# Performance work log

Hardware: AMD Instinct MI355X
Metric: run time of the kernel (lower is better)

## Reference

```python
import jax, jax.numpy as jnp
import numpy as np

N = 50000        # nodes
E = 800000       # edges (avg degree 16)
NODE_DIM = 64
HID = 64
OUT = 1
K = 2            # hops per TAGConv
P = 0.5          # dropout rate


def setup_inputs() -> dict:
    key = jax.random.key(0)
    ks = jax.random.split(key, 8)
    x = jax.random.normal(ks[0], (N, NODE_DIM), dtype=jnp.float32)
    edge_index = jax.random.randint(ks[1], (2, E), 0, N, dtype=jnp.int64)
    # positive edge weights (traffic-style), keeps degree normalization well-defined
    edge_attr = jax.random.uniform(ks[2], (E,), dtype=jnp.float32, minval=0.1, maxval=1.0)
    s = 0.1
    W0 = (jax.random.normal(ks[3], (K + 1, NODE_DIM, HID), dtype=jnp.float32) * s)
    W1 = (jax.random.normal(ks[4], (K + 1, HID, HID), dtype=jnp.float32) * s)
    W2 = (jax.random.normal(ks[5], (K + 1, HID, OUT), dtype=jnp.float32) * s)
    a0 = jnp.full((1,), 0.25, dtype=jnp.float32)  # PReLU slope (num_parameters=1)
    a1 = jnp.full((1,), 0.25, dtype=jnp.float32)
    return {"x": x, "edge_index": edge_index, "edge_attr": edge_attr,
            "W0": W0, "W1": W1, "W2": W2, "a0": a0, "a1": a1}


def _tagconv(x, row, col, norm, W):
    # out = sum_{k=0..K} (A_norm^k x) @ W[k]
    out = x @ W[0]
    h = x
    for k in range(1, K + 1):
        # gather source features, scale by edge norm, scatter-add to targets
        h = jax.ops.segment_sum(h[row] * norm[:, None], col, num_segments=N)
        out = out + h @ W[k]
    return out


def _dropout(h, key):
    keep = jax.random.bernoulli(key, 1.0 - P, h.shape)
    return jnp.where(keep, h / (1.0 - P), 0.0)


def _prelu(h, a):
    return jnp.where(h >= 0, h, a * h)


def reference(x, edge_index, edge_attr, W0, W1, W2, a0, a1):
    row, col = edge_index[0], edge_index[1]
    # symmetric GCN normalization (PyG TAGConv default, no added self-loops)
    deg = jax.ops.segment_sum(edge_attr, col, num_segments=N)
    dinv = jnp.where(deg > 0, jax.lax.rsqrt(jnp.maximum(deg, 1e-12)), 0.0)
    norm = dinv[row] * edge_attr * dinv[col]

    dk = jax.random.split(jax.random.key(42), 2)
    h = _tagconv(x, row, col, norm, W0)
    h = _prelu(_dropout(h, dk[0]), a0)
    h = _tagconv(h, row, col, norm, W1)
    h = _prelu(_dropout(h, dk[1]), a1)
    return _tagconv(h, row, col, norm, W2)
```

## Files before the change

kernel.cpp:

```cpp
#include <hip/hip_runtime.h>
#include <stdint.h>

#define N_NODES 50000
#define N_EDGES 800000
#define DIM 64
#define FEAT_TOTAL (N_NODES * DIM)
#define ELL_S 48
#define NB 200
#define BROWS 250
#define BCAP 6000
#define ECHUNK (N_EDGES / NB)
#define AST 200

typedef __attribute__((ext_vector_type(8))) short bf16x8;
typedef __attribute__((ext_vector_type(4))) float f32x4;

__device__ inline float bf2f(uint32_t h) { return __uint_as_float(h << 16); }
__device__ inline uint32_t f2bf(float f) {
  uint32_t u = __float_as_uint(f);
  return (u + 0x7fffu + ((u >> 16) & 1u)) >> 16;
}

__host__ __device__ inline void threefry2x32(uint32_t k0, uint32_t k1,
                                             uint32_t x0, uint32_t x1,
                                             uint32_t& o0, uint32_t& o1) {
  uint32_t ks[3] = {k0, k1, k0 ^ k1 ^ 0x1BD11BDAu};
  x0 += ks[0];
  x1 += ks[1];
  const uint32_t R[2][4] = {{13u, 15u, 26u, 6u}, {17u, 29u, 16u, 24u}};
#pragma unroll
  for (int g = 0; g < 5; ++g) {
    const uint32_t* r = R[g & 1];
#pragma unroll
    for (int j = 0; j < 4; ++j) {
      x0 += x1;
      x1 = (x1 << r[j]) | (x1 >> (32u - r[j]));
      x1 ^= x0;
    }
    x0 += ks[(g + 1) % 3];
    x1 += ks[(g + 2) % 3] + (uint32_t)(g + 1);
  }
  o0 = x0;
  o1 = x1;
}

__global__ __launch_bounds__(256) void phaseA(
    const int* __restrict__ row, const int* __restrict__ col,
    const float* __restrict__ w, int* __restrict__ bfill,
    int2* __restrict__ bkt, int E) {
  __shared__ int hist[NB], base[NB], off[NB];
  int t = threadIdx.x;
  int lo = blockIdx.x * ECHUNK;
  int hi = min(lo + ECHUNK, E);
  for (int i = t; i < NB; i += 256) hist[i] = 0;
  __syncthreads();
  for (int e = lo + t; e < hi; e += 256) atomicAdd(&hist[col[e] / BROWS], 1);
  __syncthreads();
  for (int i = t; i < NB; i += 256) {
    base[i] = atomicAdd(&bfill[i], hist[i]);
    off[i] = 0;
  }
  __syncthreads();
  for (int e = lo + t; e < hi; e += 256) {
    int c = col[e];
    int bin = c / BROWS;
    int rank = atomicAdd(&off[bin], 1);
    int dest = base[bin] + rank;
    if (dest < BCAP) {
      int2 ent;
      ent.x = row[e] | ((c - bin * BROWS) << 17);
      ent.y = __float_as_int(w[e]);
      bkt[(size_t)bin * BCAP + dest] = ent;
    }
  }
}

__global__ __launch_bounds__(256) void phaseC(
    const int* __restrict__ bfill, const int2* __restrict__ bkt,
    int2* __restrict__ ell, int* __restrict__ cnt, float* __restrict__ dinv) {
  __shared__ int lcnt[BROWS];
  __shared__ float ldeg[BROWS];
  int t = threadIdx.x;
  int b = blockIdx.x;
  for (int i = t; i < BROWS; i += 256) {
    lcnt[i] = 0;
    ldeg[i] = 0.0f;
  }
  __syncthreads();
  int sz = min(bfill[b], BCAP);
  const int2* src = bkt + (size_t)b * BCAP;
  for (int i = t; i < sz; i += 256) {
    int2 ent = src[i];
    int cl = (ent.x >> 17) & 0xff;
    int r = ent.x & 0x1ffff;
    float wv = __int_as_float(ent.y);
    int slot = atomicAdd(&lcnt[cl], 1);
    if (slot < ELL_S) {
      int2 o;
      o.x = r;
      o.y = ent.y;
      ell[(size_t)(b * BROWS + cl) * ELL_S + slot] = o;
    }
    atomicAdd(&ldeg[cl], wv);
  }
  __syncthreads();
  for (int i = t; i < BROWS; i += 256) {
    cnt[b * BROWS + i] = lcnt[i];
    float d = ldeg[i];
    dinv[b * BROWS + i] = (d > 0.0f) ? rsqrtf(fmaxf(d, 1e-12f)) : 0.0f;
  }
}

__global__ void normw_ell(int2* __restrict__ ell, const int* __restrict__ cnt,
                          const float* __restrict__ dinv, int n_nodes) {
  int gid = blockIdx.x * blockDim.x + threadIdx.x;
  int n = gid >> 6;
  if (n >= n_nodes) return;
  int lane = threadIdx.x & 63;
  int c = min(cnt[n], ELL_S);
  if (lane >= c) return;
  float dn = dinv[n];
  int2 ent = ell[(size_t)n * ELL_S + lane];
  ent.y = __float_as_int(dinv[ent.x] * __int_as_float(ent.y) * dn);
  ell[(size_t)n * ELL_S + lane] = ent;
}

__global__ void cvt_all(const float* __restrict__ x,
                        const float* __restrict__ W0,
                        const float* __restrict__ W1,
                        uint16_t* __restrict__ xb, uint16_t* __restrict__ Wt0,
                        uint16_t* __restrict__ Wt1) {
  int id = blockIdx.x * blockDim.x + threadIdx.x;
  if (id < FEAT_TOTAL) xb[id] = (uint16_t)f2bf(x[id]);
  if (id < 192 * DIM) {
    int kk = id >> 6;
    int j = id & 63;
    Wt0[j * 192 + kk] = (uint16_t)f2bf(W0[id]);
    Wt1[j * 192 + kk] = (uint16_t)f2bf(W1[id]);
  }
}

__global__ void prop_bf16(const uint16_t* __restrict__ src,
                          uint16_t* __restrict__ dst,
                          const int2* __restrict__ ell,
                          const int* __restrict__ cnt, int n_nodes) {
  int gid = blockIdx.x * blockDim.x + threadIdx.x;
  int n = gid >> 5;
  if (n >= n_nodes) return;
  int hl = threadIdx.x & 31;
  int eg = hl >> 3;
  int fc = hl & 7;
  int c = min(cnt[n], ELL_S);
  const int2* p = ell + (size_t)n * ELL_S;
  float acc[8] = {0.f, 0.f, 0.f, 0.f, 0.f, 0.f, 0.f, 0.f};
  int k = eg;
  for (; k + 4 < c; k += 8) {
    int2 e0 = p[k];
    int2 e1 = p[k + 4];
    float w0 = __int_as_float(e0.y);
    float w1 = __int_as_float(e1.y);
    uint4 v0 = *(const uint4*)&src[e0.x * DIM + fc * 8];
    uint4 v1 = *(const uint4*)&src[e1.x * DIM + fc * 8];
    acc[0] += bf2f(v0.x & 0xffffu) * w0 + bf2f(v1.x & 0xffffu) * w1;
    acc[1] += bf2f(v0.x >> 16) * w0 + bf2f(v1.x >> 16) * w1;
    acc[2] += bf2f(v0.y & 0xffffu) * w0 + bf2f(v1.y & 0xffffu) * w1;
    acc[3] += bf2f(v0.y >> 16) * w0 + bf2f(v1.y >> 16) * w1;
    acc[4] += bf2f(v0.z & 0xffffu) * w0 + bf2f(v1.z & 0xffffu) * w1;
    acc[5] += bf2f(v0.z >> 16) * w0 + bf2f(v1.z >> 16) * w1;
    acc[6] += bf2f(v0.w & 0xffffu) * w0 + bf2f(v1.w & 0xffffu) * w1;
    acc[7] += bf2f(v0.w >> 16) * w0 + bf2f(v1.w >> 16) * w1;
  }
  if (k < c) {
    int2 e0 = p[k];
    float w0 = __int_as_float(e0.y);
    uint4 v0 = *(const uint4*)&src[e0.x * DIM + fc * 8];
    acc[0] += bf2f(v0.x & 0xffffu) * w0;
    acc[1] += bf2f(v0.x >> 16) * w0;
    acc[2] += bf2f(v0.y & 0xffffu) * w0;
    acc[3] += bf2f(v0.y >> 16) * w0;
    acc[4] += bf2f(v0.z & 0xffffu) * w0;
    acc[5] += bf2f(v0.z >> 16) * w0;
    acc[6] += bf2f(v0.w & 0xffffu) * w0;
    acc[7] += bf2f(v0.w >> 16) * w0;
  }
#pragma unroll
  for (int m = 8; m <= 16; m <<= 1) {
#pragma unroll
    for (int j = 0; j < 8; ++j) acc[j] += __shfl_xor(acc[j], m);
  }
  if (eg == 0) {
    uint4 r;
    r.x = f2bf(acc[0]) | (f2bf(acc[1]) << 16);
    r.y = f2bf(acc[2]) | (f2bf(acc[3]) << 16);
    r.z = f2bf(acc[4]) | (f2bf(acc[5]) << 16);
    r.w = f2bf(acc[6]) | (f2bf(acc[7]) << 16);
    *(uint4*)&dst[(size_t)n * DIM + fc * 8] = r;
  }
}

__global__ void sprop_add_ell(const float* __restrict__ src,
                              const float* __restrict__ addv,
                              float* __restrict__ dst,
                              const int2* __restrict__ ell,
                              const int* __restrict__ cnt, int n_nodes) {
  int n = blockIdx.x * blockDim.x + threadIdx.x;
  if (n >= n_nodes) return;
  int c = min(cnt[n], ELL_S);
  const int2* p = ell + (size_t)n * ELL_S;
  float acc = addv[n];
  for (int k = 0; k < c; ++k)
    acc += __int_as_float(p[k].y) * src[p[k].x];
  dst[n] = acc;
}

__global__ __launch_bounds__(256) void gemm3_mfma_g(
    const uint16_t* X, const uint16_t* __restrict__ P1,
    const int2* __restrict__ ell, const int* __restrict__ cnt,
    const uint16_t* __restrict__ Wt, uint16_t* out, int n_nodes, uint32_t k0,
    uint32_t k1, const float* __restrict__ a) {
  __shared__ uint16_t sA[64 * AST];
  __shared__ uint16_t sB[64 * AST];
  int t = threadIdx.x;
  int n0 = blockIdx.x * 64;
#pragma unroll
  for (int m = 0; m < 2; ++m) {
    const uint16_t* S = (m == 0) ? X : P1;
#pragma unroll
    for (int it = 0; it < 2; ++it) {
      int chunk = t + it * 256;
      int rrow = chunk >> 3;
      int cc = chunk & 7;
      int nc = min(n0 + rrow, n_nodes - 1);
      uint4 v = *(const uint4*)&S[(size_t)nc * DIM + cc * 8];
      *(uint4*)&sA[rrow * AST + m * DIM + cc * 8] = v;
    }
  }
  {
    int wv = t >> 6;
    int lane = t & 63;
    int half = lane >> 5;
    int hl = lane & 31;
    int eg = hl >> 3;
    int fc = hl & 7;
#pragma unroll
    for (int i = 0; i < 8; ++i) {
      int ln = wv * 16 + i * 2 + half;
      int nc = min(n0 + ln, n_nodes - 1);
      int c = min(cnt[nc], ELL_S);
      const int2* p = ell + (size_t)nc * ELL_S;
      float acc[8] = {0.f, 0.f, 0.f, 0.f, 0.f, 0.f, 0.f, 0.f};
      int k = eg;
      for (; k + 4 < c; k += 8) {
        int2 e0 = p[k];
        int2 e1 = p[k + 4];
        float w0 = __int_as_float(e0.y);
        float w1 = __int_as_float(e1.y);
        uint4 v0 = *(const uint4*)&P1[e0.x * DIM + fc * 8];
        uint4 v1 = *(const uint4*)&P1[e1.x * DIM + fc * 8];
        acc[0] += bf2f(v0.x & 0xffffu) * w0 + bf2f(v1.x & 0xffffu) * w1;
        acc[1] += bf2f(v0.x >> 16) * w0 + bf2f(v1.x >> 16) * w1;
        acc[2] += bf2f(v0.y & 0xffffu) * w0 + bf2f(v1.y & 0xffffu) * w1;
        acc[3] += bf2f(v0.y >> 16) * w0 + bf2f(v1.y >> 16) * w1;
        acc[4] += bf2f(v0.z & 0xffffu) * w0 + bf2f(v1.z & 0xffffu) * w1;
        acc[5] += bf2f(v0.z >> 16) * w0 + bf2f(v1.z >> 16) * w1;
        acc[6] += bf2f(v0.w & 0xffffu) * w0 + bf2f(v1.w & 0xffffu) * w1;
        acc[7] += bf2f(v0.w >> 16) * w0 + bf2f(v1.w >> 16) * w1;
      }
      if (k < c) {
        int2 e0 = p[k];
        float w0 = __int_as_float(e0.y);
        uint4 v0 = *(const uint4*)&P1[e0.x * DIM + fc * 8];
        acc[0] += bf2f(v0.x & 0xffffu) * w0;
        acc[1] += bf2f(v0.x >> 16) * w0;
        acc[2] += bf2f(v0.y & 0xffffu) * w0;
        acc[3] += bf2f(v0.y >> 16) * w0;
        acc[4] += bf2f(v0.z & 0xffffu) * w0;
        acc[5] += bf2f(v0.z >> 16) * w0;
        acc[6] += bf2f(v0.w & 0xffffu) * w0;
        acc[7] += bf2f(v0.w >> 16) * w0;
      }
#pragma unroll
      for (int m = 8; m <= 16; m <<= 1) {
#pragma unroll
        for (int j = 0; j < 8; ++j) acc[j] += __shfl_xor(acc[j], m);
      }
      if (eg == 0) {
        uint4 r;
        r.x = f2bf(acc[0]) | (f2bf(acc[1]) << 16);
        r.y = f2bf(acc[2]) | (f2bf(acc[3]) << 16);
        r.z = f2bf(acc[4]) | (f2bf(acc[5]) << 16);
        r.w = f2bf(acc[6]) | (f2bf(acc[7]) << 16);
        *(uint4*)&sA[ln * AST + 2 * DIM + fc * 8] = r;
      }
    }
  }
#pragma unroll
  for (int it = 0; it < 6; ++it) {
    int chunk = t + it * 256;
    int rrow = chunk / 24;
    int cc = chunk % 24;
    uint4 v = *(const uint4*)&Wt[rrow * 192 + cc * 8];
    *(uint4*)&sB[rrow * AST + cc * 8] = v;
  }
  __syncthreads();
  int wv = t >> 6;
  int lane = t & 63;
  int lm = lane & 15;
  int quad = lane >> 4;
  f32x4 acc[4] = {};
  const uint16_t* pB = &sB[(wv * 16 + lm) * AST + quad * 8];
  const uint16_t* pA = &sA[lm * AST + quad * 8];
#pragma unroll
  for (int ks = 0; ks < 6; ++ks) {
    bf16x8 bf = *(const bf16x8*)(pB + ks * 32);
#pragma unroll
    for (int rt = 0; rt < 4; ++rt) {
      bf16x8 af = *(const bf16x8*)(pA + rt * 16 * AST + ks * 32);
      acc[rt] = __builtin_amdgcn_mfma_f32_16x16x32_bf16(af, bf, acc[rt], 0, 0, 0);
    }
  }
  float al = a[0];
  int col = wv * 16 + lm;
#pragma unroll
  for (int rt = 0; rt < 4; ++rt) {
#pragma unroll
    for (int r = 0; r < 4; ++r) {
      int n = n0 + rt * 16 + quad * 4 + r;
      if (n < n_nodes) {
        float v = acc[rt][r];
        uint32_t idx = (uint32_t)(n * DIM + col);
        uint32_t o0, o1;
        threefry2x32(k0, k1, 0u, idx, o0, o1);
        v = ((o0 ^ o1) & 0x80000000u) ? 0.0f : (v + v);
        v = (v >= 0.0f) ? v : al * v;
        out[(size_t)n * DIM + col] = (uint16_t)f2bf(v);
      }
    }
  }
}

__global__ void matvec3_bf16(const uint16_t* __restrict__ F,
                             const float* __restrict__ W2,
                             float* __restrict__ y0, float* __restrict__ y1,
                             float* __restrict__ y2, int n_nodes) {
  int gid = blockIdx.x * blockDim.x + threadIdx.x;
  int n = gid >> 6;
  int i = gid & 63;
  if (n >= n_nodes) return;
  float v = bf2f((uint32_t)F[(size_t)n * DIM + i]);
  float s0 = v * W2[i], s1 = v * W2[DIM + i], s2 = v * W2[2 * DIM + i];
#pragma unroll
  for (int off = 32; off > 0; off >>= 1) {
    s0 += __shfl_down(s0, off);
    s1 += __shfl_down(s1, off);
    s2 += __shfl_down(s2, off);
  }
  if (i == 0) {
    y0[n] = s0;
    y1[n] = s1;
    y2[n] = s2;
  }
}

extern "C" void kernel_launch(void* const* d_in, const int* in_sizes, int n_in,
                              void* d_out, int out_size, void* d_ws,
                              size_t ws_size, hipStream_t stream) {
  const float* x = (const float*)d_in[0];
  const int* ei = (const int*)d_in[1];
  const float* ew = (const float*)d_in[2];
  const float* W0 = (const float*)d_in[3];
  const float* W1 = (const float*)d_in[4];
  const float* W2 = (const float*)d_in[5];
  const float* a0 = (const float*)d_in[6];
  const float* a1 = (const float*)d_in[7];
  float* out = (float*)d_out;

  const int* row = ei;
  const int* col = ei + N_EDGES;

  const size_t need = (size_t)(2 * N_NODES + 256) * 4 +
                      (size_t)NB * BCAP * 8 + (size_t)N_NODES * ELL_S * 8 +
                      (size_t)(2 * 192 * DIM) * 2 +
                      (size_t)(3 * FEAT_TOTAL) * 2 + (size_t)(4 * N_NODES) * 4;
  if (ws_size < need) return;
  float* dinv = (float*)d_ws;
  int* cnt = (int*)(dinv + N_NODES);
  int* bfill = cnt + N_NODES;
  int2* bkt = (int2*)(bfill + 256);
  int2* ell = bkt + (size_t)NB * BCAP;
  uint16_t* Wt0 = (uint16_t*)(ell + (size_t)N_NODES * ELL_S);
  uint16_t* Wt1 = Wt0 + 192 * DIM;
  uint16_t* xb = Wt1 + 192 * DIM;
  uint16_t* F0 = xb + FEAT_TOTAL;
  uint16_t* F1 = F0 + FEAT_TOTAL;
  float* y0 = (float*)(F1 + FEAT_TOTAL);
  float* y1 = y0 + N_NODES;
  float* y2 = y1 + N_NODES;
  float* z1 = y2 + N_NODES;

  uint32_t dk0_0, dk0_1, dk1_0, dk1_1;
  threefry2x32(0u, 42u, 0u, 0u, dk0_0, dk0_1);
  threefry2x32(0u, 42u, 0u, 1u, dk1_0, dk1_1);

  const int BLK = 256;
  const int gridN = (N_NODES + BLK - 1) / BLK;
  const int gridNF = (FEAT_TOTAL + BLK - 1) / BLK;
  const int gridNH = (N_NODES * 32 + BLK - 1) / BLK;
  const int gridT = (N_NODES + 63) / 64;

  hipMemsetAsync(bfill, 0, 256 * sizeof(int), stream);
  phaseA<<<NB, BLK, 0, stream>>>(row, col, ew, bfill, bkt, N_EDGES);
  phaseC<<<NB, BLK, 0, stream>>>(bfill, bkt, ell, cnt, dinv);
  normw_ell<<<gridNF, BLK, 0, stream>>>(ell, cnt, dinv, N_NODES);
  cvt_all<<<gridNF, BLK, 0, stream>>>(x, W0, W1, xb, Wt0, Wt1);

  prop_bf16<<<gridNH, BLK, 0, stream>>>(xb, F1, ell, cnt, N_NODES);
  gemm3_mfma_g<<<gridT, BLK, 0, stream>>>(xb, F1, ell, cnt, Wt0, F0, N_NODES,
                                          dk0_0, dk0_1, a0);
  prop_bf16<<<gridNH, BLK, 0, stream>>>(F0, F1, ell, cnt, N_NODES);
  gemm3_mfma_g<<<gridT, BLK, 0, stream>>>(F0, F1, ell, cnt, Wt1, F0, N_NODES,
                                          dk1_0, dk1_1, a1);
  matvec3_bf16<<<gridNF, BLK, 0, stream>>>(F0, W2, y0, y1, y2, N_NODES);
  sprop_add_ell<<<gridN, BLK, 0, stream>>>(y2, y1, z1, ell, cnt, N_NODES);
  sprop_add_ell<<<gridN, BLK, 0, stream>>>(z1, y0, out, ell, cnt, N_NODES);
}
```

Measured before the change: 301.5 us.

## Unfuse second-hop propagation from MFMA GEMM and keep weights in registers

The second sparse propagation hop, previously computed inside the GEMM kernel by gathering neighbor rows into shared memory, now runs as a separate prop_bf16 launch writing a new F2 buffer. The GEMM then only loads X, P1 and P2 tiles. The weight fragments are read straight from global memory into registers rather than staged through a second shared array. This trades an extra kernel launch and an extra feature-buffer round trip for a simpler, better-occupied GEMM and better parallelism in the gather.

```diff
diff --git a/kernel.cpp b/kernel.cpp
--- a/kernel.cpp
+++ b/kernel.cpp
@@ -213,18 +213,27 @@
   dst[n] = acc;
 }
 
-__global__ __launch_bounds__(256) void gemm3_mfma_g(
+__global__ __launch_bounds__(256) void gemm3_mfma(
     const uint16_t* X, const uint16_t* __restrict__ P1,
-    const int2* __restrict__ ell, const int* __restrict__ cnt,
-    const uint16_t* __restrict__ Wt, uint16_t* out, int n_nodes, uint32_t k0,
-    uint32_t k1, const float* __restrict__ a) {
+    const uint16_t* __restrict__ P2, const uint16_t* __restrict__ Wt,
+    uint16_t* out, int n_nodes, uint32_t k0, uint32_t k1,
+    const float* __restrict__ a) {
   __shared__ uint16_t sA[64 * AST];
-  __shared__ uint16_t sB[64 * AST];
   int t = threadIdx.x;
   int n0 = blockIdx.x * 64;
-#pragma unroll
-  for (int m = 0; m < 2; ++m) {
-    const uint16_t* S = (m == 0) ? X : P1;
+  int wv = t >> 6;
+  int lane = t & 63;
+  int lm = lane & 15;
+  int quad = lane >> 4;
+  bf16x8 bfrag[6];
+  {
+    const uint16_t* pB = &Wt[(wv * 16 + lm) * 192 + quad * 8];
+#pragma unroll
+    for (int ks = 0; ks < 6; ++ks) bfrag[ks] = *(const bf16x8*)(pB + ks * 32);
+  }
+#pragma unroll
+  for (int m = 0; m < 3; ++m) {
+    const uint16_t* S = (m == 0) ? X : ((m == 1) ? P1 : P2);
 #pragma unroll
     for (int it = 0; it < 2; ++it) {
       int chunk = t + it * 256;
@@ -235,88 +244,16 @@
       *(uint4*)&sA[rrow * AST + m * DIM + cc * 8] = v;
     }
   }
-  {
-    int wv = t >> 6;
-    int lane = t & 63;
-    int half = lane >> 5;
-    int hl = lane & 31;
-    int eg = hl >> 3;
-    int fc = hl & 7;
-#pragma unroll
-    for (int i = 0; i < 8; ++i) {
-      int ln = wv * 16 + i * 2 + half;
-      int nc = min(n0 + ln, n_nodes - 1);
-      int c = min(cnt[nc], ELL_S);
-      const int2* p = ell + (size_t)nc * ELL_S;
-      float acc[8] = {0.f, 0.f, 0.f, 0.f, 0.f, 0.f, 0.f, 0.f};
-      int k = eg;
-      for (; k + 4 < c; k += 8) {
-        int2 e0 = p[k];
-        int2 e1 = p[k + 4];
-        float w0 = __int_as_float(e0.y);
-        float w1 = __int_as_float(e1.y);
-        uint4 v0 = *(const uint4*)&P1[e0.x * DIM + fc * 8];
-        uint4 v1 = *(const uint4*)&P1[e1.x * DIM + fc * 8];
-        acc[0] += bf2f(v0.x & 0xffffu) * w0 + bf2f(v1.x & 0xffffu) * w1;
-        acc[1] += bf2f(v0.x >> 16) * w0 + bf2f(v1.x >> 16) * w1;
-        acc[2] += bf2f(v0.y & 0xffffu) * w0 + bf2f(v1.y & 0xffffu) * w1;
-        acc[3] += bf2f(v0.y >> 16) * w0 + bf2f(v1.y >> 16) * w1;
-        acc[4] += bf2f(v0.z & 0xffffu) * w0 + bf2f(v1.z & 0xffffu) * w1;
-        acc[5] += bf2f(v0.z >> 16) * w0 + bf2f(v1.z >> 16) * w1;
-        acc[6] += bf2f(v0.w & 0xffffu) * w0 + bf2f(v1.w & 0xffffu) * w1;
-        acc[7] += bf2f(v0.w >> 16) * w0 + bf2f(v1.w >> 16) * w1;
-      }
-      if (k < c) {
-        int2 e0 = p[k];
-        float w0 = __int_as_float(e0.y);
-        uint4 v0 = *(const uint4*)&P1[e0.x * DIM + fc * 8];
-        acc[0] += bf2f(v0.x & 0xffffu) * w0;
-        acc[1] += bf2f(v0.x >> 16) * w0;
-        acc[2] += bf2f(v0.y & 0xffffu) * w0;
-        acc[3] += bf2f(v0.y >> 16) * w0;
-        acc[4] += bf2f(v0.z & 0xffffu) * w0;
-        acc[5] += bf2f(v0.z >> 16) * w0;
-        acc[6] += bf2f(v0.w & 0xffffu) * w0;
-        acc[7] += bf2f(v0.w >> 16) * w0;
-      }
-#pragma unroll
-      for (int m = 8; m <= 16; m <<= 1) {
-#pragma unroll
-        for (int j = 0; j < 8; ++j) acc[j] += __shfl_xor(acc[j], m);
-      }
-      if (eg == 0) {
-        uint4 r;
-        r.x = f2bf(acc[0]) | (f2bf(acc[1]) << 16);
-        r.y = f2bf(acc[2]) | (f2bf(acc[3]) << 16);
-        r.z = f2bf(acc[4]) | (f2bf(acc[5]) << 16);
-        r.w = f2bf(acc[6]) | (f2bf(acc[7]) << 16);
-        *(uint4*)&sA[ln * AST + 2 * DIM + fc * 8] = r;
-      }
-    }
-  }
-#pragma unroll
-  for (int it = 0; it < 6; ++it) {
-    int chunk = t + it * 256;
-    int rrow = chunk / 24;
-    int cc = chunk % 24;
-    uint4 v = *(const uint4*)&Wt[rrow * 192 + cc * 8];
-    *(uint4*)&sB[rrow * AST + cc * 8] = v;
-  }
-  __syncthreads();
-  int wv = t >> 6;
-  int lane = t & 63;
-  int lm = lane & 15;
-  int quad = lane >> 4;
+  __syncthreads();
   f32x4 acc[4] = {};
-  const uint16_t* pB = &sB[(wv * 16 + lm) * AST + quad * 8];
   const uint16_t* pA = &sA[lm * AST + quad * 8];
 #pragma unroll
   for (int ks = 0; ks < 6; ++ks) {
-    bf16x8 bf = *(const bf16x8*)(pB + ks * 32);
 #pragma unroll
     for (int rt = 0; rt < 4; ++rt) {
       bf16x8 af = *(const bf16x8*)(pA + rt * 16 * AST + ks * 32);
-      acc[rt] = __builtin_amdgcn_mfma_f32_16x16x32_bf16(af, bf, acc[rt], 0, 0, 0);
+      acc[rt] =
+          __builtin_amdgcn_mfma_f32_16x16x32_bf16(af, bfrag[ks], acc[rt], 0, 0, 0);
     }
   }
   float al = a[0];
@@ -381,7 +318,7 @@
   const size_t need = (size_t)(2 * N_NODES + 256) * 4 +
                       (size_t)NB * BCAP * 8 + (size_t)N_NODES * ELL_S * 8 +
                       (size_t)(2 * 192 * DIM) * 2 +
-                      (size_t)(3 * FEAT_TOTAL) * 2 + (size_t)(4 * N_NODES) * 4;
+                      (size_t)(4 * FEAT_TOTAL) * 2 + (size_t)(4 * N_NODES) * 4;
   if (ws_size < need) return;
   float* dinv = (float*)d_ws;
   int* cnt = (int*)(dinv + N_NODES);
@@ -393,7 +330,8 @@
   uint16_t* xb = Wt1 + 192 * DIM;
   uint16_t* F0 = xb + FEAT_TOTAL;
   uint16_t* F1 = F0 + FEAT_TOTAL;
-  float* y0 = (float*)(F1 + FEAT_TOTAL);
+  uint16_t* F2 = F1 + FEAT_TOTAL;
+  float* y0 = (float*)(F2 + FEAT_TOTAL);
   float* y1 = y0 + N_NODES;
   float* y2 = y1 + N_NODES;
   float* z1 = y2 + N_NODES;
@@ -415,11 +353,13 @@
   cvt_all<<<gridNF, BLK, 0, stream>>>(x, W0, W1, xb, Wt0, Wt1);
 
   prop_bf16<<<gridNH, BLK, 0, stream>>>(xb, F1, ell, cnt, N_NODES);
-  gemm3_mfma_g<<<gridT, BLK, 0, stream>>>(xb, F1, ell, cnt, Wt0, F0, N_NODES,
-                                          dk0_0, dk0_1, a0);
+  prop_bf16<<<gridNH, BLK, 0, stream>>>(F1, F2, ell, cnt, N_NODES);
+  gemm3_mfma<<<gridT, BLK, 0, stream>>>(xb, F1, F2, Wt0, F0, N_NODES, dk0_0,
+                                        dk0_1, a0);
   prop_bf16<<<gridNH, BLK, 0, stream>>>(F0, F1, ell, cnt, N_NODES);
-  gemm3_mfma_g<<<gridT, BLK, 0, stream>>>(F0, F1, ell, cnt, Wt1, F0, N_NODES,
-                                          dk1_0, dk1_1, a1);
+  prop_bf16<<<gridNH, BLK, 0, stream>>>(F1, F2, ell, cnt, N_NODES);
+  gemm3_mfma<<<gridT, BLK, 0, stream>>>(F0, F1, F2, Wt1, F0, N_NODES, dk1_0,
+                                        dk1_1, a1);
   matvec3_bf16<<<gridNF, BLK, 0, stream>>>(F0, W2, y0, y1, y2, N_NODES);
   sprop_add_ell<<<gridN, BLK, 0, stream>>>(y2, y1, z1, ell, cnt, N_NODES);
   sprop_add_ell<<<gridN, BLK, 0, stream>>>(z1, y0, out, ell, cnt, N_NODES);
```

Result: faster. 251.8 us (-16.5%).
